# Performance work log

Measured on AMD Instinct MI355X. Metric: run time of the kernel, lower is better.

The kernel has to match this reference:

```python
import jax, jax.numpy as jnp
import numpy as np

PAD = 0
B, P, ENC = 64, 196, 2048
L, V, H, E, A = 20, 32000, 512, 512, 512


def setup_inputs() -> dict:
    key = jax.random.key(0)
    ks = jax.random.split(key, 24)
    enc_out = jax.random.normal(ks[0], (B, P, ENC), dtype=jnp.float32)
    # captions: random tokens in [3, V) with variable lengths in [5, L]; sample 0 has full length L
    lengths = jax.random.randint(ks[1], (B,), 5, L + 1)
    lengths = lengths.at[0].set(L)
    toks = jax.random.randint(ks[2], (B, L), 3, V)
    pos = jnp.arange(L)
    y = jnp.where(pos[None, :] < lengths[:, None], toks, PAD).astype(jnp.int64)
    s = lambda k, shp, sc: (jax.random.normal(k, shp, dtype=jnp.float32) * sc)
    return {
        "encoder_output": enc_out,
        "y_encodings": y,
        "embed_table": jax.random.uniform(ks[3], (V, E), minval=-0.1, maxval=0.1, dtype=jnp.float32),
        "enc2att_W": s(ks[4], (A, ENC), 0.02),
        "hidden2att_W": s(ks[5], (A, H), 0.04),
        "att_W": s(ks[6], (1, A), 0.06),
        "att_b": jnp.zeros((1,), jnp.float32),
        "f_beta_W": s(ks[7], (ENC, H), 0.03),
        "f_beta_b": jnp.zeros((ENC,), jnp.float32),
        "W_ih": s(ks[8], (4 * H, E + ENC), 0.02),
        "b_ih": jnp.zeros((4 * H,), jnp.float32),
        "W_hh": s(ks[9], (4 * H, H), 0.04),
        "b_hh": jnp.zeros((4 * H,), jnp.float32),
        "fc_W": jax.random.uniform(ks[10], (V, H), minval=-0.1, maxval=0.1, dtype=jnp.float32),
        "fc_b": jnp.zeros((V,), jnp.float32),
        "init_h_W": s(ks[11], (H, ENC), 0.03),
        "init_h_b": jnp.zeros((H,), jnp.float32),
        "init_c_W": s(ks[12], (H, ENC), 0.03),
        "init_c_b": jnp.zeros((H,), jnp.float32),
    }


def _decode(encoder_output, y_encodings, embed_table, enc2att_W, hidden2att_W,
            att_W, att_b, f_beta_W, f_beta_b, W_ih, b_ih, W_hh, b_hh,
            fc_W, fc_b, init_h_W, init_h_b, init_c_W, init_c_b):
    # sort batch by caption length (descending), as in torch
    cap_len = jnp.sum(y_encodings != PAD, axis=1)          # [B]
    sort_idx = jnp.argsort(-cap_len)                       # stable in jax
    enc = encoder_output[sort_idx]                         # [B,P,ENC]
    caps = y_encodings[sort_idx]                           # [B,L]
    dec_len = cap_len[sort_idx] - 1                        # [B]
    T = L - 1                                              # static max decode length

    embed = embed_table[caps]                              # [B,L,E]
    mean_enc = enc.mean(axis=1)                            # [B,ENC]
    h0 = mean_enc @ init_h_W.T + init_h_b
    c0 = mean_enc @ init_c_W.T + init_c_b
    att1 = jnp.einsum('bpe,ae->bpa', enc, enc2att_W)       # [B,P,A], time-invariant

    def step(carry, xs):
        h, c = carry
        emb_t, t = xs                                      # emb_t: [B,E]
        # soft attention
        att2 = h @ hidden2att_W.T                          # [B,A]
        score = jnp.einsum('bpa,a->bp', jax.nn.relu(att1 + att2[:, None, :]), att_W[0]) + att_b[0]
        alpha = jax.nn.softmax(score, axis=1)              # [B,P]
        context = jnp.einsum('bp,bpe->be', alpha, enc)     # [B,ENC]
        gate = jax.nn.sigmoid(h @ f_beta_W.T + f_beta_b)   # [B,ENC]
        ctx = gate * context
        # LSTM cell (torch gate order: i, f, g, o)
        x_in = jnp.concatenate([emb_t, ctx], axis=1)       # [B,E+ENC]
        gates = x_in @ W_ih.T + b_ih + h @ W_hh.T + b_hh   # [B,4H]
        i_g, f_g, g_g, o_g = jnp.split(gates, 4, axis=1)
        c_new = jax.nn.sigmoid(f_g) * c + jax.nn.sigmoid(i_g) * jnp.tanh(g_g)
        h_new = jax.nn.sigmoid(o_g) * jnp.tanh(c_new)
        logits = h_new @ fc_W.T + fc_b                     # [B,V]
        active = (dec_len > t)[:, None]
        h = jnp.where(active, h_new, h)
        c = jnp.where(active, c_new, c)
        preds_t = jnp.where(active, logits, 0.0)
        alpha_t = jnp.where(active, alpha, 0.0)
        return (h, c), (preds_t, alpha_t)

    xs = (jnp.swapaxes(embed, 0, 1)[:T], jnp.arange(T))
    _, (preds, alphas) = jax.lax.scan(step, (h0, c0), xs)
    predictions = jnp.swapaxes(preds, 0, 1)               # [B,T,V]
    alphas = jnp.swapaxes(alphas, 0, 1)                   # [B,T,P]
    return predictions, alphas, dec_len, sort_idx


def reference(encoder_output, y_encodings, embed_table, enc2att_W, hidden2att_W,
              att_W, att_b, f_beta_W, f_beta_b, W_ih, b_ih, W_hh, b_hh,
              fc_W, fc_b, init_h_W, init_h_b, init_c_W, init_c_b):
    return _decode(encoder_output, y_encodings, embed_table, enc2att_W, hidden2att_W,
                   att_W, att_b, f_beta_W, f_beta_b, W_ih, b_ih, W_hh, b_hh,
                   fc_W, fc_b, init_h_W, init_h_b, init_c_W, init_c_b)
```

## Files before the change

kernel.cpp:

```cpp
#include <hip/hip_runtime.h>
#include <cstdint>
#include <cstddef>

#define BB 64
#define PE 196
#define PP 208
#define ENC 2048
#define LL 20
#define TT 19
#define VV 32000
#define HH 512
#define AA 512
#define KCAT 3072
#define XROW 3072
#define MROW 1216
#define MPAD 1280

typedef __attribute__((ext_vector_type(8))) short bf16x8;
typedef __attribute__((ext_vector_type(4))) float f32x4;
typedef unsigned short u16;
typedef unsigned int u32;

__device__ __forceinline__ float bf2f(u16 s){ return __uint_as_float(((u32)s) << 16); }
__device__ __forceinline__ u16 f2bf(float f){
  u32 u = __float_as_uint(f);
  u32 r = (u + 0x7FFFu + ((u >> 16) & 1u)) >> 16;
  return (u16)r;
}
__device__ __forceinline__ f32x4 mfma16(bf16x8 a, bf16x8 b, f32x4 c){
  return __builtin_amdgcn_mfma_f32_16x16x32_bf16(a, b, c, 0, 0, 0);
}
__device__ __forceinline__ float sigm(float x){ return 1.f / (1.f + __expf(-x)); }

__device__ __forceinline__ void gl_lds16(const u16* g, u16* l){
  __builtin_amdgcn_global_load_lds(
      (const __attribute__((address_space(1))) void*)g,
      (__attribute__((address_space(3))) void*)l, 16, 0, 0);
}


__global__ void k_sort(const int* __restrict__ y, int* __restrict__ sidx, int* __restrict__ dlen,
                       float* __restrict__ out_dlen, float* __restrict__ out_sidx){
  __shared__ int cl[BB];
  int b = threadIdx.x;
  int c = 0;
  for (int l = 0; l < LL; l++) c += (y[b*LL + l] != 0);
  cl[b] = c;
  __syncthreads();
  int r = 0;
  for (int j = 0; j < BB; j++){
    int cj = cl[j];
    r += (cj > c) || (cj == c && j < b);
  }
  sidx[r] = b; dlen[r] = c - 1;
  out_sidx[r] = (float)b; out_dlen[r] = (float)(c - 1);
}

__global__ void k_cvt(u16* __restrict__ dst, const float* __restrict__ src, int n){
  int i = blockIdx.x * blockDim.x + threadIdx.x;
  int stride = gridDim.x * blockDim.x;
  for (; i < n; i += stride) dst[i] = f2bf(src[i]);
}

__global__ void k_wcat(u16* __restrict__ wcat, const float* __restrict__ wih, const float* __restrict__ whh){
  int r = blockIdx.x;
  for (int j = threadIdx.x; j < KCAT; j += 256){
    float v = (j < 2560) ? wih[(size_t)r*2560 + j] : whh[(size_t)r*HH + (j - 2560)];
    wcat[(size_t)r*KCAT + j] = f2bf(v);
  }
}

__global__ void k_gather(u16* __restrict__ encb, const float* __restrict__ enc, const int* __restrict__ sidx){
  int b = blockIdx.x, pg = blockIdx.y;
  int s = sidx[b];
  const float* src = enc + (size_t)s * PE * ENC;
  u16* dst = encb + ((size_t)b * PP + pg * 8) * ENC;
  for (int i = threadIdx.x; i < 8 * ENC; i += 256){
    int p = pg * 8 + (i >> 11);
    dst[i] = (p < PE) ? f2bf(src[(size_t)p * ENC + (i & 2047)]) : (u16)0;
  }
}

__global__ void k_mean(float* __restrict__ mean, const u16* __restrict__ encb){
  int b = blockIdx.x;
  int e = blockIdx.y * 256 + threadIdx.x;
  const u16* p = encb + (size_t)b * PP * ENC + e;
  float s = 0.f;
#pragma unroll 14
  for (int pp = 0; pp < PE; pp++) s += bf2f(p[(size_t)pp * ENC]);
  mean[b*ENC + e] = s * (1.0f / 196.0f);
}

__global__ void k_embed(u16* __restrict__ embb, const float* __restrict__ table,
                        const int* __restrict__ y, const int* __restrict__ sidx){
  int b = blockIdx.x; int s = sidx[b];
  for (int i = threadIdx.x; i < TT * HH; i += 256){
    int tt = i >> 9, j = i & 511;
    int tok = y[s*LL + tt];
    embb[((size_t)b*TT + tt)*HH + j] = f2bf(table[(size_t)tok * HH + j]);
  }
}

__global__ void k_init(u16* __restrict__ xcat, float* __restrict__ cws, const float* __restrict__ mean,
                       const float* __restrict__ hW, const float* __restrict__ hb,
                       const float* __restrict__ cW, const float* __restrict__ cb){
  int isC = blockIdx.y;
  int col = blockIdx.x * 4 + (threadIdx.x >> 6);
  int row = threadIdx.x & 63;
  const float* W = isC ? cW : hW;
  const float4* m4 = (const float4*)(mean + (size_t)row * ENC);
  const float4* w4 = (const float4*)(W + (size_t)col * ENC);
  float acc = 0.f;
#pragma unroll 8
  for (int k = 0; k < ENC/4; k++){
    float4 a = m4[k], w = w4[k];
    acc = fmaf(a.x, w.x, acc); acc = fmaf(a.y, w.y, acc);
    acc = fmaf(a.z, w.z, acc); acc = fmaf(a.w, w.w, acc);
  }
  if (isC) cws[row*HH + col] = acc + cb[col];
  else     xcat[(size_t)row*XROW + 2560 + col] = f2bf(acc + hb[col]);
}

__global__ __launch_bounds__(256, 2) void k_att1(u16* __restrict__ att1,
                                                 const u16* __restrict__ encb,
                                                 const u16* __restrict__ e2a){
  __shared__ u16 ldsA[128 * 32];
  __shared__ u16 ldsB[128 * 32];
  int tid = threadIdx.x;
  int wave = tid >> 6, lane = tid & 63, quad = lane >> 4, l15 = lane & 15, kq = quad * 8;
  int mbase = blockIdx.x * 128;
  int nbase = blockIdx.y * 128;
  int wm = (wave >> 1) * 64, wn = (wave & 1) * 64;

  int srow = tid >> 2;
  int scol = (tid & 3) * 8;
  const u16* gA0 = encb + (size_t)(mbase + srow) * ENC + scol;
  const u16* gA1 = encb + (size_t)(mbase + 64 + srow) * ENC + scol;
  const u16* gB0 = e2a  + (size_t)(nbase + srow) * ENC + scol;
  const u16* gB1 = e2a  + (size_t)(nbase + 64 + srow) * ENC + scol;
  u16* lA0 = ldsA + tid * 8;
  u16* lA1 = ldsA + 2048 + tid * 8;
  u16* lB0 = ldsB + tid * 8;
  u16* lB1 = ldsB + 2048 + tid * 8;

  f32x4 acc[4][4] = {};
  for (int k0 = 0; k0 < ENC; k0 += 32){
    gl_lds16(gA0 + k0, lA0);
    gl_lds16(gA1 + k0, lA1);
    gl_lds16(gB0 + k0, lB0);
    gl_lds16(gB1 + k0, lB1);
    __syncthreads();
    bf16x8 af[4], bfr[4];
#pragma unroll
    for (int i = 0; i < 4; i++) af[i]  = *(const bf16x8*)(ldsA + (wm + i*16 + l15) * 32 + kq);
#pragma unroll
    for (int j = 0; j < 4; j++) bfr[j] = *(const bf16x8*)(ldsB + (wn + j*16 + l15) * 32 + kq);
#pragma unroll
    for (int i = 0; i < 4; i++)
#pragma unroll
      for (int j = 0; j < 4; j++)
        acc[i][j] = mfma16(af[i], bfr[j], acc[i][j]);
    __syncthreads();
  }
#pragma unroll
  for (int i = 0; i < 4; i++)
#pragma unroll
    for (int j = 0; j < 4; j++)
#pragma unroll
      for (int r = 0; r < 4; r++){
        int m = mbase + wm + i*16 + quad*4 + r;
        int n = nbase + wn + j*16 + l15;
        att1[(size_t)m * AA + n] = f2bf(acc[i][j][r]);
      }
}


__global__ void k_hmat(float* __restrict__ att2, float* __restrict__ gatelin,
                       const u16* __restrict__ xcat, const u16* __restrict__ whcat){
  int lane = threadIdx.x, quad = lane >> 4, l15 = lane & 15, kq = quad * 8;
  int n = blockIdx.x * 16 + l15;
  const u16* bp = whcat + (size_t)n * HH + kq;
  f32x4 acc[4] = {};
#pragma unroll 4
  for (int k0 = 0; k0 < HH; k0 += 32){
    bf16x8 bv = *(const bf16x8*)(bp + k0);
#pragma unroll
    for (int mt = 0; mt < 4; mt++){
      bf16x8 av = *(const bf16x8*)(xcat + (size_t)(mt*16 + l15)*XROW + 2560 + kq + k0);
      acc[mt] = mfma16(av, bv, acc[mt]);
    }
  }
#pragma unroll
  for (int mt = 0; mt < 4; mt++)
#pragma unroll
    for (int r = 0; r < 4; r++){
      int m = mt*16 + quad*4 + r;
      float v = acc[mt][r];
      if (n < HH) att2[m*HH + n] = v;
      else        gatelin[m*ENC + (n - HH)] = v;
    }
}

__global__ __launch_bounds__(256) void k_sctx(
    float* __restrict__ out_alph, float* __restrict__ alphw, u16* __restrict__ xcat,
    const u16* __restrict__ att1, const float* __restrict__ att2,
    const float* __restrict__ attW, const float* __restrict__ attb,
    const u16* __restrict__ embb, const int* __restrict__ dlen, int t){
  __shared__ float a2s[AA], aws[AA], red[256];
  int b = blockIdx.x, tid = threadIdx.x;
  float* oa = out_alph + ((size_t)b*TT + t) * PE;
  if (dlen[b] <= t){
    if (tid < PE) oa[tid] = 0.f;
    return;
  }
  a2s[tid] = att2[b*AA + tid]; a2s[tid+256] = att2[b*AA + tid + 256];
  aws[tid] = attW[tid];        aws[tid+256] = attW[tid + 256];
  __syncthreads();
  float sc = -3.4e38f;
  if (tid < PE){
    const u16* row = att1 + ((size_t)b*PP + tid) * AA;
    float acc = 0.f;
#pragma unroll 8
    for (int a0 = 0; a0 < AA; a0 += 8){
      bf16x8 v = *(const bf16x8*)(row + a0);
#pragma unroll
      for (int j = 0; j < 8; j++){
        float x = bf2f((u16)v[j]) + a2s[a0 + j];
        acc = fmaf(fmaxf(x, 0.f), aws[a0 + j], acc);
      }
    }
    sc = acc + attb[0];
  }
  red[tid] = sc; __syncthreads();
  for (int s = 128; s > 0; s >>= 1){ if (tid < s) red[tid] = fmaxf(red[tid], red[tid+s]); __syncthreads(); }
  float mx = red[0]; __syncthreads();
  float ex = (tid < PE) ? __expf(sc - mx) : 0.f;
  red[tid] = ex; __syncthreads();
  for (int s = 128; s > 0; s >>= 1){ if (tid < s) red[tid] += red[tid+s]; __syncthreads(); }
  float inv = 1.f / red[0];
  if (tid < PE) oa[tid] = ex * inv;
  if (tid < PP) alphw[b*PP + tid] = (tid < PE) ? ex * inv : 0.f;
  if (tid < 64){
    bf16x8 ev = *(const bf16x8*)(embb + ((size_t)b*TT + t)*HH + tid*8);
    *(bf16x8*)(xcat + (size_t)b*XROW + tid*8) = ev;
  }
}

__global__ __launch_bounds__(256) void k_ctxv(
    u16* __restrict__ xcat, const u16* __restrict__ encb,
    const float* __restrict__ alphw, const float* __restrict__ gatelin,
    const float* __restrict__ fbb, const int* __restrict__ dlen, int t){
  int b = blockIdx.x;
  if (dlen[b] <= t) return;
  int yc = blockIdx.y;
  __shared__ float al[PP];
  __shared__ float red[8][32][8];
  int tid = threadIdx.x;
  if (tid < PP) al[tid] = alphw[b*PP + tid];
  __syncthreads();
  int pg = tid >> 5, tw = tid & 31;
  const u16* ep = encb + (size_t)b*PP*ENC + yc*256 + tw*8;
  float acc[8] = {};
  for (int p = pg; p < PE; p += 8){
    bf16x8 v = *(const bf16x8*)(ep + (size_t)p*ENC);
    float a = al[p];
#pragma unroll
    for (int j = 0; j < 8; j++) acc[j] = fmaf(a, bf2f((u16)v[j]), acc[j]);
  }
#pragma unroll
  for (int j = 0; j < 8; j++) red[pg][tw][j] = acc[j];
  __syncthreads();
  int tw2 = tid >> 3, j2 = tid & 7;
  float s = 0.f;
#pragma unroll
  for (int g = 0; g < 8; g++) s += red[g][tw2][j2];
  int e = yc*256 + tid;
  float gt = sigm(gatelin[b*ENC + e] + fbb[e]);
  xcat[(size_t)b*XROW + 512 + e] = f2bf(gt * s);
}

__global__ void k_gates(u16* __restrict__ xcat, float* __restrict__ cws,
                        u16* __restrict__ hsave,
                        const u16* __restrict__ wcat,
                        const float* __restrict__ bih, const float* __restrict__ bhh,
                        const int* __restrict__ dlen, int t){
  __shared__ float red[4][16][64];
  int tid = threadIdx.x;
  int wave = tid >> 6, lane = tid & 63, quad = lane >> 4, l15 = lane & 15, kq = quad * 8;
  int col = blockIdx.x*16 + l15;
  int mb = blockIdx.y * 16;
  int kbase = wave * 768;
  const u16* ap = xcat + (size_t)(mb + l15)*XROW + kbase + kq;
  const u16* b0p = wcat + (size_t)(col)       *KCAT + kbase + kq;
  const u16* b1p = wcat + (size_t)(512 + col) *KCAT + kbase + kq;
  const u16* b2p = wcat + (size_t)(1024 + col)*KCAT + kbase + kq;
  const u16* b3p = wcat + (size_t)(1536 + col)*KCAT + kbase + kq;
  f32x4 a0 = {}, a1 = {}, a2 = {}, a3 = {};
#pragma unroll 4
  for (int k0 = 0; k0 < 768; k0 += 32){
    bf16x8 a  = *(const bf16x8*)(ap + k0);
    bf16x8 b0 = *(const bf16x8*)(b0p + k0);
    bf16x8 b1 = *(const bf16x8*)(b1p + k0);
    bf16x8 b2 = *(const bf16x8*)(b2p + k0);
    bf16x8 b3 = *(const bf16x8*)(b3p + k0);
    a0 = mfma16(a, b0, a0); a1 = mfma16(a, b1, a1);
    a2 = mfma16(a, b2, a2); a3 = mfma16(a, b3, a3);
  }
#pragma unroll
  for (int r = 0; r < 4; r++){
    red[wave][r][lane]      = a0[r];
    red[wave][4 + r][lane]  = a1[r];
    red[wave][8 + r][lane]  = a2[r];
    red[wave][12 + r][lane] = a3[r];
  }
  __syncthreads();
  if (wave == 0){
    float g0[4], g1[4], g2[4], g3[4];
#pragma unroll
    for (int r = 0; r < 4; r++){
      g0[r] = red[0][r][lane]      + red[1][r][lane]      + red[2][r][lane]      + red[3][r][lane];
      g1[r] = red[0][4+r][lane]    + red[1][4+r][lane]    + red[2][4+r][lane]    + red[3][4+r][lane];
      g2[r] = red[0][8+r][lane]    + red[1][8+r][lane]    + red[2][8+r][lane]    + red[3][8+r][lane];
      g3[r] = red[0][12+r][lane]   + red[1][12+r][lane]   + red[2][12+r][lane]   + red[3][12+r][lane];
    }
    float bi0 = bih[col]      + bhh[col];
    float bi1 = bih[512+col]  + bhh[512+col];
    float bi2 = bih[1024+col] + bhh[1024+col];
    float bi3 = bih[1536+col] + bhh[1536+col];
#pragma unroll
    for (int r = 0; r < 4; r++){
      int m = mb + quad*4 + r;
      if (dlen[m] > t){
        float gi = g0[r] + bi0, gf = g1[r] + bi1, gg = g2[r] + bi2, go = g3[r] + bi3;
        float cn = sigm(gf) * cws[m*HH + col] + sigm(gi) * tanhf(gg);
        cws[m*HH + col] = cn;
        u16 hb = f2bf(sigm(go) * tanhf(cn));
        xcat[(size_t)m*XROW + 2560 + col] = hb;
        hsave[((size_t)m*TT + t)*HH + col] = hb;
      }
    }
  }
}

__global__ __launch_bounds__(256, 2) void k_fcall(float* __restrict__ out,
                                                  const u16* __restrict__ hsave,
                                                  const u16* __restrict__ fcw,
                                                  const float* __restrict__ fcb,
                                                  const int* __restrict__ dlen){
  const int nwg = (MPAD/128) * (VV/128);
  const int q = nwg >> 3, r = nwg & 7;
  int id = blockIdx.x;
  int xcd = id & 7, local = id >> 3;
  int wgid = (xcd < r ? xcd*(q+1) : r*(q+1) + (xcd-r)*q) + local;
  int mt = wgid % (MPAD/128);
  int nt = wgid / (MPAD/128);

  __shared__ u16 ldsA[128 * 32];
  __shared__ u16 ldsB[128 * 32];
  __shared__ float ldsc[32 * 129];
  int tid = threadIdx.x;
  int wave = tid >> 6, lane = tid & 63, quad = lane >> 4, l15 = lane & 15, kq = quad * 8;
  int mbase = mt * 128;
  int nbase = nt * 128;
  int wm = (wave >> 1) * 64, wn = (wave & 1) * 64;

  int srow = tid >> 2;
  int scol = (tid & 3) * 8;
  const u16* gA0 = hsave + (size_t)(mbase + srow) * HH + scol;
  const u16* gA1 = hsave + (size_t)(mbase + 64 + srow) * HH + scol;
  const u16* gB0 = fcw + (size_t)(nbase + srow) * HH + scol;
  const u16* gB1 = fcw + (size_t)(nbase + 64 + srow) * HH + scol;
  u16* lA0 = ldsA + tid * 8;
  u16* lA1 = ldsA + 2048 + tid * 8;
  u16* lB0 = ldsB + tid * 8;
  u16* lB1 = ldsB + 2048 + tid * 8;

  f32x4 acc[4][4] = {};
  for (int k0 = 0; k0 < HH; k0 += 32){
    gl_lds16(gA0 + k0, lA0);
    gl_lds16(gA1 + k0, lA1);
    gl_lds16(gB0 + k0, lB0);
    gl_lds16(gB1 + k0, lB1);
    __syncthreads();
    bf16x8 af[4], bfr[4];
#pragma unroll
    for (int i = 0; i < 4; i++) af[i]  = *(const bf16x8*)(ldsA + (wm + i*16 + l15) * 32 + kq);
#pragma unroll
    for (int j = 0; j < 4; j++) bfr[j] = *(const bf16x8*)(ldsB + (wn + j*16 + l15) * 32 + kq);
#pragma unroll
    for (int i = 0; i < 4; i++)
#pragma unroll
      for (int j = 0; j < 4; j++)
        acc[i][j] = mfma16(af[i], bfr[j], acc[i][j]);
    __syncthreads();
  }

  int c4 = (tid & 31) * 4;
  float4 bias = *(const float4*)(fcb + nbase + c4);

#pragma unroll
  for (int i = 0; i < 4; i++){
#pragma unroll
    for (int j = 0; j < 4; j++)
#pragma unroll
      for (int r2 = 0; r2 < 4; r2++){
        int rb = (wave >> 1) * 16 + quad * 4 + r2;
        int cb = wn + j*16 + l15;
        ldsc[rb * 129 + cb] = acc[i][j][r2];
      }
    __syncthreads();
#pragma unroll
    for (int k = 0; k < 4; k++){
      int rb = (tid >> 5) + k * 8;
      float4 v = *(const float4*)(ldsc + rb * 129 + c4);
      int m = mbase + (rb >> 4) * 64 + i * 16 + (rb & 15);
      if (m < MROW){
        int b = m / TT, t = m - b * TT;
        bool act = dlen[b] > t;
        float4 o;
        o.x = act ? v.x + bias.x : 0.f;
        o.y = act ? v.y + bias.y : 0.f;
        o.z = act ? v.z + bias.z : 0.f;
        o.w = act ? v.w + bias.w : 0.f;
        *(float4*)(out + (size_t)m * VV + nbase + c4) = o;
      }
    }
    __syncthreads();
  }
}

extern "C" void kernel_launch(void* const* d_in, const int* in_sizes, int n_in,
                              void* d_out, int out_size, void* d_ws, size_t ws_size,
                              hipStream_t stream){
  const float* enc  = (const float*)d_in[0];
  const int*   y    = (const int*)  d_in[1];
  const float* etab = (const float*)d_in[2];
  const float* e2aW = (const float*)d_in[3];
  const float* h2aW = (const float*)d_in[4];
  const float* attW = (const float*)d_in[5];
  const float* attb = (const float*)d_in[6];
  const float* fbW  = (const float*)d_in[7];
  const float* fbb  = (const float*)d_in[8];
  const float* wih  = (const float*)d_in[9];
  const float* bih  = (const float*)d_in[10];
  const float* whh  = (const float*)d_in[11];
  const float* bhh  = (const float*)d_in[12];
  const float* fcW  = (const float*)d_in[13];
  const float* fcb  = (const float*)d_in[14];
  const float* ihW  = (const float*)d_in[15];
  const float* ihb  = (const float*)d_in[16];
  const float* icW  = (const float*)d_in[17];
  const float* icb  = (const float*)d_in[18];

  char* ws = (char*)d_ws;
  size_t off = 0;
  auto alloc = [&](size_t bytes){ void* p = ws + off; off += (bytes + 255) & ~(size_t)255; return p; };
  u16* encb    = (u16*)alloc((size_t)BB*PP*ENC*2);
  u16* att1    = (u16*)alloc((size_t)BB*PP*AA*2);
  u16* fcwb    = (u16*)alloc((size_t)VV*HH*2);
  u16* wcat    = (u16*)alloc((size_t)2048*KCAT*2);
  u16* whcat   = (u16*)alloc((size_t)2560*HH*2);
  u16* e2ab    = (u16*)alloc((size_t)AA*ENC*2);
  u16* embb    = (u16*)alloc((size_t)BB*TT*HH*2);
  u16* xcat    = (u16*)alloc((size_t)BB*XROW*2);
  u16* hsave   = (u16*)alloc((size_t)MPAD*HH*2);
  float* att2  = (float*)alloc((size_t)BB*AA*4);
  float* gatel = (float*)alloc((size_t)BB*ENC*4);
  float* alphw = (float*)alloc((size_t)BB*PP*4);
  float* cws   = (float*)alloc((size_t)BB*HH*4);
  float* mean  = (float*)alloc((size_t)BB*ENC*4);
  int* sidx    = (int*)alloc(BB*4);
  int* dlen    = (int*)alloc(BB*4);

  float* out      = (float*)d_out;
  float* out_alph = out + (size_t)BB*TT*VV;
  float* out_dlen = out_alph + (size_t)BB*TT*PE;
  float* out_sidx = out_dlen + BB;

  k_sort<<<1, 64, 0, stream>>>(y, sidx, dlen, out_dlen, out_sidx);
  k_cvt<<<2048, 256, 0, stream>>>(e2ab, e2aW, AA*ENC);
  k_cvt<<<2048, 256, 0, stream>>>(whcat, h2aW, AA*HH);
  k_cvt<<<2048, 256, 0, stream>>>(whcat + (size_t)AA*HH, fbW, ENC*HH);
  k_cvt<<<2048, 256, 0, stream>>>(fcwb, fcW, VV*HH);
  k_wcat<<<2048, 256, 0, stream>>>(wcat, wih, whh);
  k_gather<<<dim3(64, 26), 256, 0, stream>>>(encb, enc, sidx);
  k_mean<<<dim3(64, 8), 256, 0, stream>>>(mean, encb);
  k_embed<<<64, 256, 0, stream>>>(embb, etab, y, sidx);
  k_init<<<dim3(128, 2), 256, 0, stream>>>(xcat, cws, mean, ihW, ihb, icW, icb);
  k_att1<<<dim3(104, 4), 256, 0, stream>>>(att1, encb, e2ab);

  for (int t = 0; t < TT; t++){
    k_hmat<<<160, 64, 0, stream>>>(att2, gatel, xcat, whcat);
    k_sctx<<<64, 256, 0, stream>>>(out_alph, alphw, xcat, att1, att2, attW, attb,
                                   embb, dlen, t);
    k_ctxv<<<dim3(64, 8), 256, 0, stream>>>(xcat, encb, alphw, gatel, fbb, dlen, t);
    k_gates<<<dim3(32, 4), 256, 0, stream>>>(xcat, cws, hsave, wcat, bih, bhh, dlen, t);
  }
  k_fcall<<<(MPAD/128)*(VV/128), 256, 0, stream>>>(out, hsave, fcwb, fcb, dlen);
}
```

Before: 1.691 ms.

## Fuse per-timestep decoder kernels into one persistent cooperative kernel with grid syncs

Replaces the 76 per-timestep kernel launches (hmat, sctx, ctxv, gates over 19 steps) with a single cooperative persistent kernel. Inside it, blocks loop over the work items of each stage and use grid-wide syncs between stages. The goal is to remove launch overhead and the gaps between dependent kernels. The costs are grid barrier latency, fewer blocks (up to 512) with combined shared memory that may cut occupancy, and a fallback to the old path if the cooperative launch fails.

```diff
diff --git a/kernel.cpp b/kernel.cpp
--- a/kernel.cpp
+++ b/kernel.cpp
@@ -1,6 +1,9 @@
 #include <hip/hip_runtime.h>
+#include <hip/hip_cooperative_groups.h>
 #include <cstdint>
 #include <cstddef>
+
+namespace cg = cooperative_groups;
 
 #define BB 64
 #define PE 196
@@ -175,10 +178,12 @@
 }
 
 
-__global__ void k_hmat(float* __restrict__ att2, float* __restrict__ gatelin,
-                       const u16* __restrict__ xcat, const u16* __restrict__ whcat){
-  int lane = threadIdx.x, quad = lane >> 4, l15 = lane & 15, kq = quad * 8;
-  int n = blockIdx.x * 16 + l15;
+__device__ __forceinline__ void hmat_job(
+    int gw, int lane,
+    float* __restrict__ att2, float* __restrict__ gatelin,
+    const u16* __restrict__ xcat, const u16* __restrict__ whcat){
+  int quad = lane >> 4, l15 = lane & 15, kq = quad * 8;
+  int n = gw * 16 + l15;
   const u16* bp = whcat + (size_t)n * HH + kq;
   f32x4 acc[4] = {};
 #pragma unroll 4
@@ -201,20 +206,20 @@
     }
 }
 
-__global__ __launch_bounds__(256) void k_sctx(
+__device__ __forceinline__ void sctx_job(
+    int b, int t, int tid,
     float* __restrict__ out_alph, float* __restrict__ alphw, u16* __restrict__ xcat,
     const u16* __restrict__ att1, const float* __restrict__ att2,
     const float* __restrict__ attW, const float* __restrict__ attb,
-    const u16* __restrict__ embb, const int* __restrict__ dlen, int t){
-  __shared__ float a2s[AA], aws[AA], red[256];
-  int b = blockIdx.x, tid = threadIdx.x;
+    const u16* __restrict__ embb, const int* __restrict__ dlen,
+    float* s_a2, float* s_aw, float* s_red){
   float* oa = out_alph + ((size_t)b*TT + t) * PE;
   if (dlen[b] <= t){
     if (tid < PE) oa[tid] = 0.f;
     return;
   }
-  a2s[tid] = att2[b*AA + tid]; a2s[tid+256] = att2[b*AA + tid + 256];
-  aws[tid] = attW[tid];        aws[tid+256] = attW[tid + 256];
+  s_a2[tid] = att2[b*AA + tid]; s_a2[tid+256] = att2[b*AA + tid + 256];
+  s_aw[tid] = attW[tid];        s_aw[tid+256] = attW[tid + 256];
   __syncthreads();
   float sc = -3.4e38f;
   if (tid < PE){
@@ -225,19 +230,19 @@
       bf16x8 v = *(const bf16x8*)(row + a0);
 #pragma unroll
       for (int j = 0; j < 8; j++){
-        float x = bf2f((u16)v[j]) + a2s[a0 + j];
-        acc = fmaf(fmaxf(x, 0.f), aws[a0 + j], acc);
+        float x = bf2f((u16)v[j]) + s_a2[a0 + j];
+        acc = fmaf(fmaxf(x, 0.f), s_aw[a0 + j], acc);
       }
     }
     sc = acc + attb[0];
   }
-  red[tid] = sc; __syncthreads();
-  for (int s = 128; s > 0; s >>= 1){ if (tid < s) red[tid] = fmaxf(red[tid], red[tid+s]); __syncthreads(); }
-  float mx = red[0]; __syncthreads();
+  s_red[tid] = sc; __syncthreads();
+  for (int s = 128; s > 0; s >>= 1){ if (tid < s) s_red[tid] = fmaxf(s_red[tid], s_red[tid+s]); __syncthreads(); }
+  float mx = s_red[0]; __syncthreads();
   float ex = (tid < PE) ? __expf(sc - mx) : 0.f;
-  red[tid] = ex; __syncthreads();
-  for (int s = 128; s > 0; s >>= 1){ if (tid < s) red[tid] += red[tid+s]; __syncthreads(); }
-  float inv = 1.f / red[0];
+  s_red[tid] = ex; __syncthreads();
+  for (int s = 128; s > 0; s >>= 1){ if (tid < s) s_red[tid] += s_red[tid+s]; __syncthreads(); }
+  float inv = 1.f / s_red[0];
   if (tid < PE) oa[tid] = ex * inv;
   if (tid < PP) alphw[b*PP + tid] = (tid < PE) ? ex * inv : 0.f;
   if (tid < 64){
@@ -246,49 +251,45 @@
   }
 }
 
-__global__ __launch_bounds__(256) void k_ctxv(
+__device__ __forceinline__ void ctxv_job(
+    int b, int yc, int t, int tid,
     u16* __restrict__ xcat, const u16* __restrict__ encb,
     const float* __restrict__ alphw, const float* __restrict__ gatelin,
-    const float* __restrict__ fbb, const int* __restrict__ dlen, int t){
-  int b = blockIdx.x;
+    const float* __restrict__ fbb, const int* __restrict__ dlen,
+    float* s_al, float (*s_cred)[32][8]){
   if (dlen[b] <= t) return;
-  int yc = blockIdx.y;
-  __shared__ float al[PP];
-  __shared__ float red[8][32][8];
-  int tid = threadIdx.x;
-  if (tid < PP) al[tid] = alphw[b*PP + tid];
+  if (tid < PP) s_al[tid] = alphw[b*PP + tid];
   __syncthreads();
   int pg = tid >> 5, tw = tid & 31;
   const u16* ep = encb + (size_t)b*PP*ENC + yc*256 + tw*8;
   float acc[8] = {};
   for (int p = pg; p < PE; p += 8){
     bf16x8 v = *(const bf16x8*)(ep + (size_t)p*ENC);
-    float a = al[p];
+    float a = s_al[p];
 #pragma unroll
     for (int j = 0; j < 8; j++) acc[j] = fmaf(a, bf2f((u16)v[j]), acc[j]);
   }
 #pragma unroll
-  for (int j = 0; j < 8; j++) red[pg][tw][j] = acc[j];
+  for (int j = 0; j < 8; j++) s_cred[pg][tw][j] = acc[j];
   __syncthreads();
   int tw2 = tid >> 3, j2 = tid & 7;
   float s = 0.f;
 #pragma unroll
-  for (int g = 0; g < 8; g++) s += red[g][tw2][j2];
+  for (int g = 0; g < 8; g++) s += s_cred[g][tw2][j2];
   int e = yc*256 + tid;
   float gt = sigm(gatelin[b*ENC + e] + fbb[e]);
   xcat[(size_t)b*XROW + 512 + e] = f2bf(gt * s);
 }
 
-__global__ void k_gates(u16* __restrict__ xcat, float* __restrict__ cws,
-                        u16* __restrict__ hsave,
-                        const u16* __restrict__ wcat,
-                        const float* __restrict__ bih, const float* __restrict__ bhh,
-                        const int* __restrict__ dlen, int t){
-  __shared__ float red[4][16][64];
-  int tid = threadIdx.x;
+__device__ __forceinline__ void gates_job(
+    int nx, int my, int t, int tid,
+    u16* __restrict__ xcat, float* __restrict__ cws, u16* __restrict__ hsave,
+    const u16* __restrict__ wcat,
+    const float* __restrict__ bih, const float* __restrict__ bhh,
+    const int* __restrict__ dlen, float (*s_gred)[16][64]){
   int wave = tid >> 6, lane = tid & 63, quad = lane >> 4, l15 = lane & 15, kq = quad * 8;
-  int col = blockIdx.x*16 + l15;
-  int mb = blockIdx.y * 16;
+  int col = nx*16 + l15;
+  int mb = my * 16;
   int kbase = wave * 768;
   const u16* ap = xcat + (size_t)(mb + l15)*XROW + kbase + kq;
   const u16* b0p = wcat + (size_t)(col)       *KCAT + kbase + kq;
@@ -308,20 +309,20 @@
   }
 #pragma unroll
   for (int r = 0; r < 4; r++){
-    red[wave][r][lane]      = a0[r];
-    red[wave][4 + r][lane]  = a1[r];
-    red[wave][8 + r][lane]  = a2[r];
-    red[wave][12 + r][lane] = a3[r];
+    s_gred[wave][r][lane]      = a0[r];
+    s_gred[wave][4 + r][lane]  = a1[r];
+    s_gred[wave][8 + r][lane]  = a2[r];
+    s_gred[wave][12 + r][lane] = a3[r];
   }
   __syncthreads();
   if (wave == 0){
     float g0[4], g1[4], g2[4], g3[4];
 #pragma unroll
     for (int r = 0; r < 4; r++){
-      g0[r] = red[0][r][lane]      + red[1][r][lane]      + red[2][r][lane]      + red[3][r][lane];
-      g1[r] = red[0][4+r][lane]    + red[1][4+r][lane]    + red[2][4+r][lane]    + red[3][4+r][lane];
-      g2[r] = red[0][8+r][lane]    + red[1][8+r][lane]    + red[2][8+r][lane]    + red[3][8+r][lane];
-      g3[r] = red[0][12+r][lane]   + red[1][12+r][lane]   + red[2][12+r][lane]   + red[3][12+r][lane];
+      g0[r] = s_gred[0][r][lane]    + s_gred[1][r][lane]    + s_gred[2][r][lane]    + s_gred[3][r][lane];
+      g1[r] = s_gred[0][4+r][lane]  + s_gred[1][4+r][lane]  + s_gred[2][4+r][lane]  + s_gred[3][4+r][lane];
+      g2[r] = s_gred[0][8+r][lane]  + s_gred[1][8+r][lane]  + s_gred[2][8+r][lane]  + s_gred[3][8+r][lane];
+      g3[r] = s_gred[0][12+r][lane] + s_gred[1][12+r][lane] + s_gred[2][12+r][lane] + s_gred[3][12+r][lane];
     }
     float bi0 = bih[col]      + bhh[col];
     float bi1 = bih[512+col]  + bhh[512+col];
@@ -339,6 +340,87 @@
         hsave[((size_t)m*TT + t)*HH + col] = hb;
       }
     }
+  }
+}
+
+
+__global__ void k_hmat(float* __restrict__ att2, float* __restrict__ gatelin,
+                       const u16* __restrict__ xcat, const u16* __restrict__ whcat){
+  hmat_job(blockIdx.x, threadIdx.x, att2, gatelin, xcat, whcat);
+}
+
+__global__ __launch_bounds__(256) void k_sctx(
+    float* __restrict__ out_alph, float* __restrict__ alphw, u16* __restrict__ xcat,
+    const u16* __restrict__ att1, const float* __restrict__ att2,
+    const float* __restrict__ attW, const float* __restrict__ attb,
+    const u16* __restrict__ embb, const int* __restrict__ dlen, int t){
+  __shared__ float s_a2[AA], s_aw[AA], s_red[256];
+  sctx_job(blockIdx.x, t, threadIdx.x, out_alph, alphw, xcat, att1, att2,
+           attW, attb, embb, dlen, s_a2, s_aw, s_red);
+}
+
+__global__ __launch_bounds__(256) void k_ctxv(
+    u16* __restrict__ xcat, const u16* __restrict__ encb,
+    const float* __restrict__ alphw, const float* __restrict__ gatelin,
+    const float* __restrict__ fbb, const int* __restrict__ dlen, int t){
+  __shared__ float s_al[PP];
+  __shared__ float s_cred[8][32][8];
+  ctxv_job(blockIdx.x, blockIdx.y, t, threadIdx.x, xcat, encb, alphw, gatelin,
+           fbb, dlen, s_al, s_cred);
+}
+
+__global__ void k_gates(u16* __restrict__ xcat, float* __restrict__ cws,
+                        u16* __restrict__ hsave, const u16* __restrict__ wcat,
+                        const float* __restrict__ bih, const float* __restrict__ bhh,
+                        const int* __restrict__ dlen, int t){
+  __shared__ float s_gred[4][16][64];
+  gates_job(blockIdx.x, blockIdx.y, t, threadIdx.x, xcat, cws, hsave, wcat,
+            bih, bhh, dlen, s_gred);
+}
+
+__global__ __launch_bounds__(256, 2) void k_loop(
+    float* __restrict__ out_alph, float* __restrict__ alphw, u16* __restrict__ xcat,
+    float* __restrict__ att2, float* __restrict__ gatel, float* __restrict__ cws,
+    u16* __restrict__ hsave,
+    const u16* __restrict__ att1, const u16* __restrict__ encb,
+    const u16* __restrict__ wcat, const u16* __restrict__ whcat,
+    const u16* __restrict__ embb,
+    const float* __restrict__ attW, const float* __restrict__ attb,
+    const float* __restrict__ fbb,
+    const float* __restrict__ bih, const float* __restrict__ bhh,
+    const int* __restrict__ dlen){
+  cg::grid_group gg = cg::this_grid();
+  const int G = gridDim.x;
+  const int tid = threadIdx.x;
+  const int wave = tid >> 6, lane = tid & 63;
+
+  __shared__ float s_a2[AA], s_aw[AA], s_red[256];
+  __shared__ float s_al[PP];
+  __shared__ float s_cred[8][32][8];
+  __shared__ float s_gred[4][16][64];
+
+  for (int t = 0; t < TT; t++){
+    for (int gw = blockIdx.x * 4 + wave; gw < 160; gw += G * 4)
+      hmat_job(gw, lane, att2, gatel, xcat, whcat);
+    gg.sync();
+    for (int b = blockIdx.x; b < BB; b += G){
+      sctx_job(b, t, tid, out_alph, alphw, xcat, att1, att2, attW, attb,
+               embb, dlen, s_a2, s_aw, s_red);
+      __syncthreads();
+    }
+    gg.sync();
+    for (int job = blockIdx.x; job < BB*8; job += G){
+      ctxv_job(job >> 3, job & 7, t, tid, xcat, encb, alphw, gatel, fbb, dlen,
+               s_al, s_cred);
+      __syncthreads();
+    }
+    gg.sync();
+    for (int job = blockIdx.x; job < 128; job += G){
+      gates_job(job & 31, job >> 5, t, tid, xcat, cws, hsave, wcat, bih, bhh,
+                dlen, s_gred);
+      __syncthreads();
+    }
+    gg.sync();
   }
 }
 
@@ -489,12 +571,32 @@
   k_init<<<dim3(128, 2), 256, 0, stream>>>(xcat, cws, mean, ihW, ihb, icW, icb);
   k_att1<<<dim3(104, 4), 256, 0, stream>>>(att1, encb, e2ab);
 
-  for (int t = 0; t < TT; t++){
-    k_hmat<<<160, 64, 0, stream>>>(att2, gatel, xcat, whcat);
-    k_sctx<<<64, 256, 0, stream>>>(out_alph, alphw, xcat, att1, att2, attW, attb,
-                                   embb, dlen, t);
-    k_ctxv<<<dim3(64, 8), 256, 0, stream>>>(xcat, encb, alphw, gatel, fbb, dlen, t);
-    k_gates<<<dim3(32, 4), 256, 0, stream>>>(xcat, cws, hsave, wcat, bih, bhh, dlen, t);
+  static int coopGrid = 0;
+  if (coopGrid == 0){
+    int nb = 0;
+    if (hipOccupancyMaxActiveBlocksPerMultiprocessor(&nb, k_loop, 256, 0) != hipSuccess || nb < 1)
+      nb = 1;
+    int g = nb * 256;
+    if (g > 512) g = 512;
+    coopGrid = g;
+  }
+  {
+    float* oa = out_alph;
+    void* args[] = { &oa, &alphw, &xcat, &att2, &gatel, &cws, &hsave,
+                     &att1, &encb, &wcat, &whcat, &embb,
+                     (void*)&attW, (void*)&attb, (void*)&fbb,
+                     (void*)&bih, (void*)&bhh, &dlen };
+    hipError_t ce = hipLaunchCooperativeKernel(k_loop, dim3(coopGrid), dim3(256),
+                                               args, 0, stream);
+    if (ce != hipSuccess){
+      for (int t = 0; t < TT; t++){
+        k_hmat<<<160, 64, 0, stream>>>(att2, gatel, xcat, whcat);
+        k_sctx<<<64, 256, 0, stream>>>(out_alph, alphw, xcat, att1, att2, attW, attb,
+                                       embb, dlen, t);
+        k_ctxv<<<dim3(64, 8), 256, 0, stream>>>(xcat, encb, alphw, gatel, fbb, dlen, t);
+        k_gates<<<dim3(32, 4), 256, 0, stream>>>(xcat, cws, hsave, wcat, bih, bhh, dlen, t);
+      }
+    }
   }
   k_fcall<<<(MPAD/128)*(VV/128), 256, 0, stream>>>(out, hsave, fcwb, fcb, dlen);
 }
```

After: 3.854 ms. +128.0%, slower.

## Fuse hidden matvec, attention softmax and context into one per-step kernel

Applied to the files above, without the earlier changes.

Replaces the three per-step kernels (MFMA hidden-projection GEMM, attention score/softmax, context-vector gating) with a single k_step kernel launched on a 64x8 grid. Each block recomputes the hidden-to-attention projection with scalar FMAs and redoes the score softmax for its batch row. Intermediate global buffers (att2, gatelin, alphw) disappear, along with two launches per timestep. The cost is that the 512x512 projection and the attention scores are computed redundantly in all 8 column blocks. Weight rows are also read per thread with a stride instead of through coalesced MFMA loads, which adds L2 traffic and ALU work.

```diff
diff --git a/kernel.cpp b/kernel.cpp
--- a/kernel.cpp
+++ b/kernel.cpp
@@ -175,47 +175,55 @@
 }
 
 
-__global__ void k_hmat(float* __restrict__ att2, float* __restrict__ gatelin,
-                       const u16* __restrict__ xcat, const u16* __restrict__ whcat){
-  int lane = threadIdx.x, quad = lane >> 4, l15 = lane & 15, kq = quad * 8;
-  int n = blockIdx.x * 16 + l15;
-  const u16* bp = whcat + (size_t)n * HH + kq;
-  f32x4 acc[4] = {};
-#pragma unroll 4
-  for (int k0 = 0; k0 < HH; k0 += 32){
-    bf16x8 bv = *(const bf16x8*)(bp + k0);
-#pragma unroll
-    for (int mt = 0; mt < 4; mt++){
-      bf16x8 av = *(const bf16x8*)(xcat + (size_t)(mt*16 + l15)*XROW + 2560 + kq + k0);
-      acc[mt] = mfma16(av, bv, acc[mt]);
-    }
-  }
-#pragma unroll
-  for (int mt = 0; mt < 4; mt++)
-#pragma unroll
-    for (int r = 0; r < 4; r++){
-      int m = mt*16 + quad*4 + r;
-      float v = acc[mt][r];
-      if (n < HH) att2[m*HH + n] = v;
-      else        gatelin[m*ENC + (n - HH)] = v;
-    }
-}
-
-__global__ __launch_bounds__(256) void k_sctx(
-    float* __restrict__ out_alph, float* __restrict__ alphw, u16* __restrict__ xcat,
-    const u16* __restrict__ att1, const float* __restrict__ att2,
+__global__ __launch_bounds__(256) void k_step(
+    float* __restrict__ out_alph, u16* __restrict__ xcat,
+    const u16* __restrict__ att1, const u16* __restrict__ encb,
+    const u16* __restrict__ whcat, const u16* __restrict__ embb,
     const float* __restrict__ attW, const float* __restrict__ attb,
-    const u16* __restrict__ embb, const int* __restrict__ dlen, int t){
-  __shared__ float a2s[AA], aws[AA], red[256];
-  int b = blockIdx.x, tid = threadIdx.x;
+    const float* __restrict__ fbb, const int* __restrict__ dlen, int t){
+  int b = blockIdx.x, yc = blockIdx.y, tid = threadIdx.x;
   float* oa = out_alph + ((size_t)b*TT + t) * PE;
   if (dlen[b] <= t){
-    if (tid < PE) oa[tid] = 0.f;
+    if (yc == 0 && tid < PE) oa[tid] = 0.f;
     return;
   }
-  a2s[tid] = att2[b*AA + tid]; a2s[tid+256] = att2[b*AA + tid + 256];
-  aws[tid] = attW[tid];        aws[tid+256] = attW[tid + 256];
-  __syncthreads();
+  __shared__ float s_h[HH];
+  __shared__ float s_a2[AA];
+  __shared__ float s_aw[AA];
+  __shared__ float s_red[256];
+  __shared__ float s_al[PP];
+  __shared__ float s_cred[8][32][8];
+
+  s_h[tid]       = bf2f(xcat[(size_t)b*XROW + 2560 + tid]);
+  s_h[tid + 256] = bf2f(xcat[(size_t)b*XROW + 2560 + tid + 256]);
+  s_aw[tid] = attW[tid]; s_aw[tid + 256] = attW[tid + 256];
+  __syncthreads();
+
+  int e = yc*256 + tid;
+  float gl;
+  {
+    const u16* w0 = whcat + (size_t)tid * HH;
+    const u16* w1 = whcat + (size_t)(tid + 256) * HH;
+    const u16* w2 = whcat + (size_t)(512 + e) * HH;
+    float a0 = 0.f, a1 = 0.f, a2 = 0.f;
+#pragma unroll 4
+    for (int k = 0; k < HH; k += 8){
+      bf16x8 v0 = *(const bf16x8*)(w0 + k);
+      bf16x8 v1 = *(const bf16x8*)(w1 + k);
+      bf16x8 v2 = *(const bf16x8*)(w2 + k);
+#pragma unroll
+      for (int j = 0; j < 8; j++){
+        float hh = s_h[k + j];
+        a0 = fmaf(hh, bf2f((u16)v0[j]), a0);
+        a1 = fmaf(hh, bf2f((u16)v1[j]), a1);
+        a2 = fmaf(hh, bf2f((u16)v2[j]), a2);
+      }
+    }
+    s_a2[tid] = a0; s_a2[tid + 256] = a1;
+    gl = a2 + fbb[e];
+  }
+  __syncthreads();
+
   float sc = -3.4e38f;
   if (tid < PE){
     const u16* row = att1 + ((size_t)b*PP + tid) * AA;
@@ -225,58 +233,45 @@
       bf16x8 v = *(const bf16x8*)(row + a0);
 #pragma unroll
       for (int j = 0; j < 8; j++){
-        float x = bf2f((u16)v[j]) + a2s[a0 + j];
-        acc = fmaf(fmaxf(x, 0.f), aws[a0 + j], acc);
+        float x = bf2f((u16)v[j]) + s_a2[a0 + j];
+        acc = fmaf(fmaxf(x, 0.f), s_aw[a0 + j], acc);
       }
     }
     sc = acc + attb[0];
   }
-  red[tid] = sc; __syncthreads();
-  for (int s = 128; s > 0; s >>= 1){ if (tid < s) red[tid] = fmaxf(red[tid], red[tid+s]); __syncthreads(); }
-  float mx = red[0]; __syncthreads();
+  s_red[tid] = sc; __syncthreads();
+  for (int s = 128; s > 0; s >>= 1){ if (tid < s) s_red[tid] = fmaxf(s_red[tid], s_red[tid+s]); __syncthreads(); }
+  float mx = s_red[0]; __syncthreads();
   float ex = (tid < PE) ? __expf(sc - mx) : 0.f;
-  red[tid] = ex; __syncthreads();
-  for (int s = 128; s > 0; s >>= 1){ if (tid < s) red[tid] += red[tid+s]; __syncthreads(); }
-  float inv = 1.f / red[0];
-  if (tid < PE) oa[tid] = ex * inv;
-  if (tid < PP) alphw[b*PP + tid] = (tid < PE) ? ex * inv : 0.f;
-  if (tid < 64){
-    bf16x8 ev = *(const bf16x8*)(embb + ((size_t)b*TT + t)*HH + tid*8);
-    *(bf16x8*)(xcat + (size_t)b*XROW + tid*8) = ev;
-  }
-}
-
-__global__ __launch_bounds__(256) void k_ctxv(
-    u16* __restrict__ xcat, const u16* __restrict__ encb,
-    const float* __restrict__ alphw, const float* __restrict__ gatelin,
-    const float* __restrict__ fbb, const int* __restrict__ dlen, int t){
-  int b = blockIdx.x;
-  if (dlen[b] <= t) return;
-  int yc = blockIdx.y;
-  __shared__ float al[PP];
-  __shared__ float red[8][32][8];
-  int tid = threadIdx.x;
-  if (tid < PP) al[tid] = alphw[b*PP + tid];
-  __syncthreads();
+  s_red[tid] = ex; __syncthreads();
+  for (int s = 128; s > 0; s >>= 1){ if (tid < s) s_red[tid] += s_red[tid+s]; __syncthreads(); }
+  float inv = 1.f / s_red[0];
+  if (tid < PP) s_al[tid] = (tid < PE) ? ex * inv : 0.f;
+  if (yc == 0){
+    if (tid < PE) oa[tid] = ex * inv;
+    if (tid < 64){
+      bf16x8 ev = *(const bf16x8*)(embb + ((size_t)b*TT + t)*HH + tid*8);
+      *(bf16x8*)(xcat + (size_t)b*XROW + tid*8) = ev;
+    }
+  }
+  __syncthreads();
+
   int pg = tid >> 5, tw = tid & 31;
   const u16* ep = encb + (size_t)b*PP*ENC + yc*256 + tw*8;
   float acc[8] = {};
   for (int p = pg; p < PE; p += 8){
     bf16x8 v = *(const bf16x8*)(ep + (size_t)p*ENC);
-    float a = al[p];
+    float a = s_al[p];
 #pragma unroll
     for (int j = 0; j < 8; j++) acc[j] = fmaf(a, bf2f((u16)v[j]), acc[j]);
   }
 #pragma unroll
-  for (int j = 0; j < 8; j++) red[pg][tw][j] = acc[j];
-  __syncthreads();
-  int tw2 = tid >> 3, j2 = tid & 7;
+  for (int j = 0; j < 8; j++) s_cred[pg][tw][j] = acc[j];
+  __syncthreads();
   float s = 0.f;
 #pragma unroll
-  for (int g = 0; g < 8; g++) s += red[g][tw2][j2];
-  int e = yc*256 + tid;
-  float gt = sigm(gatelin[b*ENC + e] + fbb[e]);
-  xcat[(size_t)b*XROW + 512 + e] = f2bf(gt * s);
+  for (int g = 0; g < 8; g++) s += s_cred[g][tid >> 3][tid & 7];
+  xcat[(size_t)b*XROW + 512 + e] = f2bf(sigm(gl) * s);
 }
 
 __global__ void k_gates(u16* __restrict__ xcat, float* __restrict__ cws,
@@ -464,9 +459,6 @@
   u16* embb    = (u16*)alloc((size_t)BB*TT*HH*2);
   u16* xcat    = (u16*)alloc((size_t)BB*XROW*2);
   u16* hsave   = (u16*)alloc((size_t)MPAD*HH*2);
-  float* att2  = (float*)alloc((size_t)BB*AA*4);
-  float* gatel = (float*)alloc((size_t)BB*ENC*4);
-  float* alphw = (float*)alloc((size_t)BB*PP*4);
   float* cws   = (float*)alloc((size_t)BB*HH*4);
   float* mean  = (float*)alloc((size_t)BB*ENC*4);
   int* sidx    = (int*)alloc(BB*4);
@@ -490,10 +482,8 @@
   k_att1<<<dim3(104, 4), 256, 0, stream>>>(att1, encb, e2ab);
 
   for (int t = 0; t < TT; t++){
-    k_hmat<<<160, 64, 0, stream>>>(att2, gatel, xcat, whcat);
-    k_sctx<<<64, 256, 0, stream>>>(out_alph, alphw, xcat, att1, att2, attW, attb,
-                                   embb, dlen, t);
-    k_ctxv<<<dim3(64, 8), 256, 0, stream>>>(xcat, encb, alphw, gatel, fbb, dlen, t);
+    k_step<<<dim3(64, 8), 256, 0, stream>>>(out_alph, xcat, att1, encb, whcat,
+                                            embb, attW, attb, fbb, dlen, t);
     k_gates<<<dim3(32, 4), 256, 0, stream>>>(xcat, cws, hsave, wcat, bih, bhh, dlen, t);
   }
   k_fcall<<<(MPAD/128)*(VV/128), 256, 0, stream>>>(out, hsave, fcwb, fcb, dlen);
```

Measured after the change: 2.352 ms. +39.1%, slower.
